# Optimization experiments

Measured on AMD Instinct MI355X. Metric: run time of the kernel, lower is better.

## Reference

```python
import jax, jax.numpy as jnp
import numpy as np
from math import sqrt

MASK_SCALE = 128  # band half-width; entries with |i-j| < MASK_SCALE are masked to -inf

B, L, H, E = 4, 2048, 8, 64
D = 64


def setup_inputs() -> dict:
    key = jax.random.key(0)
    kq, kk, kv = jax.random.split(key, 3)
    queries = jax.random.normal(kq, (B, L, H, E), dtype=jnp.float32)
    keys = jax.random.normal(kk, (B, L, H, E), dtype=jnp.float32)
    values = jax.random.normal(kv, (B, L, H, D), dtype=jnp.float32)
    attn_mask = jnp.zeros((B, 1, L, L), dtype=bool)  # unused (mask_flag=False)
    return {"queries": queries, "keys": keys, "values": values, "attn_mask": attn_mask}


def reference(queries, keys, values, attn_mask):
    b, l, h, e = queries.shape
    scale = 1.0 / sqrt(e)
    # [B,H,L,S] dense scores
    scores = jnp.einsum('blhe,bshe->bhls', queries, keys)
    # create_diag_symmetric_mask(L, MASK_SCALE): 1 iff |i-j| < MASK_SCALE
    idx = jnp.arange(l)
    band = jnp.abs(idx[:, None] - idx[None, :]) < MASK_SCALE  # [L,L]
    # module masks the band to -inf (attends outside the band)
    scores = jnp.where(band[None, None, :, :], -jnp.inf, scores)
    A = jax.nn.softmax(scale * scores, axis=-1)
    V = jnp.einsum('bhls,bshd->blhd', A, values)
    return V
```

## Files before the change

### kernel.cpp

```cpp
#include <hip/hip_runtime.h>
#include <hip/hip_bf16.h>

typedef __bf16 bf16_t;
typedef __bf16 bf16x8 __attribute__((ext_vector_type(8)));
typedef float f32x4 __attribute__((ext_vector_type(4)));
typedef float f32x16 __attribute__((ext_vector_type(16)));
typedef unsigned int u32;

#define MFMA16(A,B,C) __builtin_amdgcn_mfma_f32_16x16x32_bf16(A,B,C,0,0,0)
#define MFMA32(A,B,C) __builtin_amdgcn_mfma_f32_32x32x16_bf16(A,B,C,0,0,0)

constexpr int Bb = 4, Ll = 2048, Hh = 8, Ee = 64, Dd = 64;
constexpr int LDP = 72;
constexpr int MS = 128;

static __device__ __forceinline__ bf16x8 cvt8(float4 a, float4 b) {
    bf16x8 t;
    t[0] = (bf16_t)a.x; t[1] = (bf16_t)a.y; t[2] = (bf16_t)a.z; t[3] = (bf16_t)a.w;
    t[4] = (bf16_t)b.x; t[5] = (bf16_t)b.y; t[6] = (bf16_t)b.z; t[7] = (bf16_t)b.w;
    return t;
}

static __device__ __forceinline__ u32 pkbf(float lo, float hi) {
    u32 d;
    asm("v_cvt_pk_bf16_f32 %0, %1, %2" : "=v"(d) : "v"(lo), "v"(hi));
    return d;
}

static __device__ __forceinline__ float fexp2(float x) {
    float r;
    asm("v_exp_f32 %0, %1" : "=v"(r) : "v"(x));
    return r;
}

static __device__ __forceinline__ f32x16 zero16() {
    f32x16 z;
    #pragma unroll
    for (int r = 0; r < 16; ++r) z[r] = 0.f;
    return z;
}

__global__ __launch_bounds__(256) void cvt_qk(const float* __restrict__ src,
                                              bf16_t* __restrict__ dst,
                                              float scale) {
    const int c = blockIdx.x * 256 + threadIdx.x;
    const int e0 = (c & 7) * 8;
    const int h  = (c >> 3) & (Hh - 1);
    const int l  = (c >> 6) & (Ll - 1);
    const int b  = c >> 17;
    const float* s = src + ((((size_t)b * Ll + l) * Hh + h) * Ee + e0);
    float4 f0 = ((const float4*)s)[0];
    float4 f1 = ((const float4*)s)[1];
    f0.x *= scale; f0.y *= scale; f0.z *= scale; f0.w *= scale;
    f1.x *= scale; f1.y *= scale; f1.z *= scale; f1.w *= scale;
    *(bf16x8*)(dst + ((((size_t)b * Hh + h) * Ll + l) * Ee + e0)) = cvt8(f0, f1);
}

__global__ __launch_bounds__(256) void cvt_v(const float* __restrict__ V,
                                             bf16_t* __restrict__ Vt) {
    __shared__ bf16_t VLp[Dd][LDP];
    const int bh = blockIdx.x >> 5;
    const int t  = blockIdx.x & 31;
    const int b = bh >> 3, h = bh & 7;
    {
        const int j  = threadIdx.x >> 2;
        const int d0 = (threadIdx.x & 3) * 16;
        const float* vp = V + (((size_t)(b * Ll + t * 64 + j)) * Hh + h) * Dd + d0;
        float4 x0 = ((const float4*)vp)[0], x1 = ((const float4*)vp)[1];
        float4 x2 = ((const float4*)vp)[2], x3 = ((const float4*)vp)[3];
        VLp[d0 +  0][j] = (bf16_t)x0.x; VLp[d0 +  1][j] = (bf16_t)x0.y;
        VLp[d0 +  2][j] = (bf16_t)x0.z; VLp[d0 +  3][j] = (bf16_t)x0.w;
        VLp[d0 +  4][j] = (bf16_t)x1.x; VLp[d0 +  5][j] = (bf16_t)x1.y;
        VLp[d0 +  6][j] = (bf16_t)x1.z; VLp[d0 +  7][j] = (bf16_t)x1.w;
        VLp[d0 +  8][j] = (bf16_t)x2.x; VLp[d0 +  9][j] = (bf16_t)x2.y;
        VLp[d0 + 10][j] = (bf16_t)x2.z; VLp[d0 + 11][j] = (bf16_t)x2.w;
        VLp[d0 + 12][j] = (bf16_t)x3.x; VLp[d0 + 13][j] = (bf16_t)x3.y;
        VLp[d0 + 14][j] = (bf16_t)x3.z; VLp[d0 + 15][j] = (bf16_t)x3.w;
    }
    __syncthreads();
    {
        const int d  = threadIdx.x >> 2;
        const int j0 = (threadIdx.x & 3) * 16;
        bf16x8 a0 = *(const bf16x8*)&VLp[d][j0];
        bf16x8 a1 = *(const bf16x8*)&VLp[d][j0 + 8];
        bf16_t* op = Vt + ((((size_t)bh * 32 + t) * 64 + d) * 64 + j0);
        *(bf16x8*)op = a0;
        *(bf16x8*)(op + 8) = a1;
    }
}

__global__ __launch_bounds__(256, 2) void fattn4(const float* __restrict__ Q,
                                                 const bf16_t* __restrict__ Kb,
                                                 const bf16_t* __restrict__ Vt,
                                                 float* __restrict__ O) {
    __shared__ __align__(16) bf16_t KL[2 * 4096];
    __shared__ __align__(16) bf16_t VL[2 * 4096];

    const int tid = threadIdx.x;
    const int wv  = tid >> 6;
    const int ln  = tid & 63;
    const int l31 = ln & 31;
    const int lh  = ln >> 5;

    const int bid = blockIdx.x;
    const int x   = bid & 7;
    const int o   = bid >> 3;
    const int bh  = x * 4 + (o >> 4);
    const int qt  = o & 15;
    const int q0  = qt * 128;
    const int wq0 = q0 + wv * 32;
    const int qq  = wq0 + l31;
    const int b = bh >> 3, h = bh & 7;

    const bf16_t* kbase = Kb + (size_t)bh * (Ll * 64);
    const bf16_t* vbase = Vt + (size_t)bh * (Ll * 64);

    bf16x8 qreg[4];
    {
        const float SCL2 = 0.125f * 1.44269504f;
        const float* qp = Q + (((size_t)(b * Ll + qq)) * Hh + h) * Ee + lh * 8;
        #pragma unroll
        for (int ks = 0; ks < 4; ++ks) {
            float4 f0 = *(const float4*)(qp + ks * 16);
            float4 f1 = *(const float4*)(qp + ks * 16 + 4);
            f0.x *= SCL2; f0.y *= SCL2; f0.z *= SCL2; f0.w *= SCL2;
            f1.x *= SCL2; f1.y *= SCL2; f1.z *= SCL2; f1.w *= SCL2;
            qreg[ks] = cvt8(f0, f1);
        }
    }

    bf16x8 ones;
    #pragma unroll
    for (int e = 0; e < 8; ++e) ones[e] = (bf16_t)1.0f;

    f32x16 acc0 = zero16(), acc1 = zero16(), accP = zero16();

    const int rowoff = (ln >> 3) * 64 + (((ln & 7) ^ (ln >> 3)) * 8);
    const int i0 = (wv & 1) * 4;
    const bf16_t* gsb = (wv < 2) ? kbase : vbase;
    bf16_t* lsb = (wv < 2) ? KL : VL;

    const int s0t = q0 >> 6;
    constexpr int NT = 30;

    #define STAGE(nxt, kt_) do {                                                   \
        const bf16_t* _g = gsb + (kt_) * 4096 + i0 * 512 + rowoff;                 \
        bf16_t* _l = lsb + (nxt) * 4096 + i0 * 512;                                \
        _Pragma("unroll")                                                          \
        for (int _c = 0; _c < 4; ++_c)                                             \
            __builtin_amdgcn_global_load_lds((const void*)(_g + _c * 512),         \
                                             (void*)(_l + _c * 512), 16, 0, 0);    \
    } while (0)

    STAGE(0, (0 >= s0t ? 2 : 0));

    for (int i = 0; i < NT; ++i) {
        const int kt_ = i + (i >= s0t ? 2 : 0);
        const int k0 = kt_ * 64;

        if (i + 1 < NT) {
            STAGE((i + 1) & 1, (i + 1) + ((i + 1) >= s0t ? 2 : 0));
            asm volatile("s_waitcnt vmcnt(4)" ::: "memory");
        } else {
            asm volatile("s_waitcnt vmcnt(0)" ::: "memory");
        }
        __builtin_amdgcn_s_barrier();

        const int bo = (i & 1) * 4096;

        f32x16 s0v = zero16(), s1v = zero16();
        __builtin_amdgcn_s_setprio(1);
        #pragma unroll
        for (int ks = 0; ks < 4; ++ks) {
            const int cc = (((2 * ks + lh) ^ (l31 & 7)) << 3);
            bf16x8 ka0 = *(const bf16x8*)&KL[bo + l31 * 64 + cc];
            bf16x8 ka1 = *(const bf16x8*)&KL[bo + (32 + l31) * 64 + cc];
            s0v = MFMA32(ka0, qreg[ks], s0v);
            s1v = MFMA32(ka1, qreg[ks], s1v);
        }
        __builtin_amdgcn_s_setprio(0);

        {
            const int d0_ = wq0 - k0;
            if (d0_ > -159 && d0_ < 159) {
                #pragma unroll
                for (int r = 0; r < 16; ++r) {
                    const int k = k0 + 4 * lh + ((r & 3) + 8 * (r >> 2));
                    const int dlt = qq - k;
                    if (dlt > -MS && dlt < MS) s0v[r] = -1e30f;
                }
            }
            const int d1_ = wq0 - (k0 + 32);
            if (d1_ > -159 && d1_ < 159) {
                #pragma unroll
                for (int r = 0; r < 16; ++r) {
                    const int k = k0 + 32 + 4 * lh + ((r & 3) + 8 * (r >> 2));
                    const int dlt = qq - k;
                    if (dlt > -MS && dlt < MS) s1v[r] = -1e30f;
                }
            }
        }

        bf16x8 pf[4];
        {
            float p[16];
            #pragma unroll
            for (int r = 0; r < 16; ++r) p[r] = fexp2(s0v[r]);
            u32 x0 = pkbf(p[0], p[1]),   x1 = pkbf(p[2], p[3]);
            u32 x2 = pkbf(p[4], p[5]),   x3 = pkbf(p[6], p[7]);
            u32 x4 = pkbf(p[8], p[9]),   x5 = pkbf(p[10], p[11]);
            u32 x6 = pkbf(p[12], p[13]), x7 = pkbf(p[14], p[15]);
            asm volatile("v_permlane32_swap_b32 %0, %1" : "+v"(x0), "+v"(x2));
            asm volatile("v_permlane32_swap_b32 %0, %1" : "+v"(x1), "+v"(x3));
            asm volatile("v_permlane32_swap_b32 %0, %1" : "+v"(x4), "+v"(x6));
            asm volatile("v_permlane32_swap_b32 %0, %1" : "+v"(x5), "+v"(x7));
            union { u32 w[4]; bf16x8 v; } u0, u1;
            u0.w[0] = x0; u0.w[1] = x1; u0.w[2] = x2; u0.w[3] = x3;
            u1.w[0] = x4; u1.w[1] = x5; u1.w[2] = x6; u1.w[3] = x7;
            pf[0] = u0.v; pf[1] = u1.v;
        }
        {
            float p[16];
            #pragma unroll
            for (int r = 0; r < 16; ++r) p[r] = fexp2(s1v[r]);
            u32 x0 = pkbf(p[0], p[1]),   x1 = pkbf(p[2], p[3]);
            u32 x2 = pkbf(p[4], p[5]),   x3 = pkbf(p[6], p[7]);
            u32 x4 = pkbf(p[8], p[9]),   x5 = pkbf(p[10], p[11]);
            u32 x6 = pkbf(p[12], p[13]), x7 = pkbf(p[14], p[15]);
            asm volatile("v_permlane32_swap_b32 %0, %1" : "+v"(x0), "+v"(x2));
            asm volatile("v_permlane32_swap_b32 %0, %1" : "+v"(x1), "+v"(x3));
            asm volatile("v_permlane32_swap_b32 %0, %1" : "+v"(x4), "+v"(x6));
            asm volatile("v_permlane32_swap_b32 %0, %1" : "+v"(x5), "+v"(x7));
            union { u32 w[4]; bf16x8 v; } u0, u1;
            u0.w[0] = x0; u0.w[1] = x1; u0.w[2] = x2; u0.w[3] = x3;
            u1.w[0] = x4; u1.w[1] = x5; u1.w[2] = x6; u1.w[3] = x7;
            pf[2] = u0.v; pf[3] = u1.v;
        }

        __builtin_amdgcn_s_setprio(1);
        #pragma unroll
        for (int ks = 0; ks < 4; ++ks) {
            const int cc = (((2 * ks + lh) ^ (l31 & 7)) << 3);
            bf16x8 vf0 = *(const bf16x8*)&VL[bo + l31 * 64 + cc];
            bf16x8 vf1 = *(const bf16x8*)&VL[bo + (32 + l31) * 64 + cc];
            acc0 = MFMA32(pf[ks], vf0, acc0);
            acc1 = MFMA32(pf[ks], vf1, acc1);
            accP = MFMA32(pf[ks], ones, accP);
        }
        __builtin_amdgcn_s_setprio(0);

        __builtin_amdgcn_s_barrier();
    }
    #undef STAGE

    #pragma unroll
    for (int r = 0; r < 16; ++r) {
        const int rr = (r & 3) + 8 * (r >> 2) + 4 * lh;
        const float ir = 1.0f / accP[r];
        float* op = O + ((size_t)(b * Ll + wq0 + rr) * Hh + h) * Dd + l31;
        op[0]  = acc0[r] * ir;
        op[32] = acc1[r] * ir;
    }
}

__global__ __launch_bounds__(256, 2) void fattn_f32(const float* __restrict__ Q,
                                                    const float* __restrict__ K,
                                                    const float* __restrict__ V,
                                                    float* __restrict__ O) {
    __shared__ __align__(16) bf16_t Klds[64][LDP];
    __shared__ __align__(16) bf16_t Vtlds[Dd][LDP];
    __shared__ __align__(16) bf16_t Plds[4][16][LDP];

    const int tid = threadIdx.x;
    const int wv  = tid >> 6;
    const int ln  = tid & 63;
    const int l15 = ln & 15;
    const int g   = ln >> 4;

    const int nqt = Ll / 64;
    const int bid = blockIdx.x;
    const int qt  = bid % nqt;
    const int bh  = bid / nqt;
    const int b   = bh >> 3;
    const int h   = bh & 7;
    const int q0  = qt * 64;

    const float SCL2 = 0.125f * 1.44269504f;

    bf16x8 qf[2];
    {
        const float* qp = Q + (((size_t)(b * Ll + q0 + wv * 16 + l15)) * Hh + h) * Ee + g * 8;
        #pragma unroll
        for (int ks = 0; ks < 2; ++ks) {
            float4 f0 = *(const float4*)(qp + 32 * ks);
            float4 f1 = *(const float4*)(qp + 32 * ks + 4);
            qf[ks] = cvt8(f0, f1);
        }
    }

    f32x4 acc[4];
    #pragma unroll
    for (int ct = 0; ct < 4; ++ct) acc[ct] = (f32x4){0.f, 0.f, 0.f, 0.f};
    float m2[4], lsum[4];
    #pragma unroll
    for (int r = 0; r < 4; ++r) { m2[r] = -1e30f; lsum[r] = 0.f; }

    for (int k0 = 0; k0 < Ll; k0 += 64) {
        const int dd = k0 - q0;
        if (dd >= -64 && dd <= 64) continue;
        const bool needmask = (dd == 128) || (dd == -128);

        __syncthreads();
        {
            const int j  = tid >> 2;
            const int c0 = (tid & 3) << 4;
            const float* kp = K + (((size_t)(b * Ll + k0 + j)) * Hh + h) * Ee + c0;
            const float* vp = V + (((size_t)(b * Ll + k0 + j)) * Hh + h) * Dd + c0;
            float4 a0 = ((const float4*)kp)[0], a1 = ((const float4*)kp)[1];
            float4 a2 = ((const float4*)kp)[2], a3 = ((const float4*)kp)[3];
            *(bf16x8*)&Klds[j][c0]     = cvt8(a0, a1);
            *(bf16x8*)&Klds[j][c0 + 8] = cvt8(a2, a3);
            float4 b0 = ((const float4*)vp)[0], b1 = ((const float4*)vp)[1];
            float4 b2 = ((const float4*)vp)[2], b3 = ((const float4*)vp)[3];
            Vtlds[c0 +  0][j] = (bf16_t)b0.x; Vtlds[c0 +  1][j] = (bf16_t)b0.y;
            Vtlds[c0 +  2][j] = (bf16_t)b0.z; Vtlds[c0 +  3][j] = (bf16_t)b0.w;
            Vtlds[c0 +  4][j] = (bf16_t)b1.x; Vtlds[c0 +  5][j] = (bf16_t)b1.y;
            Vtlds[c0 +  6][j] = (bf16_t)b1.z; Vtlds[c0 +  7][j] = (bf16_t)b1.w;
            Vtlds[c0 +  8][j] = (bf16_t)b2.x; Vtlds[c0 +  9][j] = (bf16_t)b2.y;
            Vtlds[c0 + 10][j] = (bf16_t)b2.z; Vtlds[c0 + 11][j] = (bf16_t)b2.w;
            Vtlds[c0 + 12][j] = (bf16_t)b3.x; Vtlds[c0 + 13][j] = (bf16_t)b3.y;
            Vtlds[c0 + 14][j] = (bf16_t)b3.z; Vtlds[c0 + 15][j] = (bf16_t)b3.w;
        }
        __syncthreads();

        f32x4 s[4];
        #pragma unroll
        for (int ct = 0; ct < 4; ++ct) {
            f32x4 z = (f32x4){0.f, 0.f, 0.f, 0.f};
            #pragma unroll
            for (int ks = 0; ks < 2; ++ks) {
                bf16x8 kf = *(const bf16x8*)&Klds[ct * 16 + l15][ks * 32 + g * 8];
                z = MFMA16(qf[ks], kf, z);
            }
            s[ct] = z;
        }

        float lg[4][4];
        #pragma unroll
        for (int ct = 0; ct < 4; ++ct)
            #pragma unroll
            for (int r = 0; r < 4; ++r)
                lg[ct][r] = s[ct][r] * SCL2;

        if (needmask) {
            const int irow = q0 + wv * 16 + g * 4;
            #pragma unroll
            for (int ct = 0; ct < 4; ++ct) {
                const int j = k0 + ct * 16 + l15;
                #pragma unroll
                for (int r = 0; r < 4; ++r) {
                    int diff = irow + r - j;
                    diff = diff < 0 ? -diff : diff;
                    if (diff < MS) lg[ct][r] = -1e30f;
                }
            }
        }

        #pragma unroll
        for (int r = 0; r < 4; ++r) {
            float mx = fmaxf(fmaxf(lg[0][r], lg[1][r]), fmaxf(lg[2][r], lg[3][r]));
            #pragma unroll
            for (int off = 1; off < 16; off <<= 1) mx = fmaxf(mx, __shfl_xor(mx, off));
            const float mnew = fmaxf(m2[r], mx);
            const float c = exp2f(m2[r] - mnew);
            m2[r] = mnew;
            #pragma unroll
            for (int ct = 0; ct < 4; ++ct) acc[ct][r] *= c;
            float ps = 0.f;
            #pragma unroll
            for (int ct = 0; ct < 4; ++ct) {
                float p = exp2f(lg[ct][r] - mnew);
                bf16_t pb = (bf16_t)p;
                Plds[wv][g * 4 + r][ct * 16 + l15] = pb;
                ps += (float)pb;
            }
            #pragma unroll
            for (int off = 1; off < 16; off <<= 1) ps += __shfl_xor(ps, off);
            lsum[r] = lsum[r] * c + ps;
        }

        __syncthreads();

        #pragma unroll
        for (int ks = 0; ks < 2; ++ks) {
            bf16x8 pfr = *(const bf16x8*)&Plds[wv][l15][ks * 32 + g * 8];
            #pragma unroll
            for (int ct = 0; ct < 4; ++ct) {
                bf16x8 vf = *(const bf16x8*)&Vtlds[ct * 16 + l15][ks * 32 + g * 8];
                acc[ct] = MFMA16(pfr, vf, acc[ct]);
            }
        }
    }

    #pragma unroll
    for (int r = 0; r < 4; ++r) {
        const float inv = 1.0f / lsum[r];
        const size_t row = (size_t)(b * Ll + q0 + wv * 16 + g * 4 + r);
        float* op = O + (row * Hh + h) * Dd;
        #pragma unroll
        for (int ct = 0; ct < 4; ++ct)
            op[ct * 16 + l15] = acc[ct][r] * inv;
    }
}

extern "C" void kernel_launch(void* const* d_in, const int* in_sizes, int n_in,
                              void* d_out, int out_size, void* d_ws, size_t ws_size,
                              hipStream_t stream) {
    const float* Q = (const float*)d_in[0];
    const float* K = (const float*)d_in[1];
    const float* V = (const float*)d_in[2];
    float* O = (float*)d_out;

    const size_t nelem = (size_t)Bb * Hh * Ll * Ee;
    const size_t need  = nelem * 2 * 2;

    if (ws_size >= need) {
        bf16_t* Kb = (bf16_t*)d_ws;
        bf16_t* Vt = Kb + nelem;
        cvt_qk<<<dim3(2048), dim3(256), 0, stream>>>(K, Kb, 1.0f);
        cvt_v<<<dim3(Bb * Hh * 32), dim3(256), 0, stream>>>(V, Vt);
        fattn4<<<dim3(512), dim3(256), 0, stream>>>(Q, Kb, Vt, O);
    } else {
        fattn_f32<<<dim3(Bb * Hh * 32), dim3(256), 0, stream>>>(Q, K, V, O);
    }
}
```

Baseline: 62.84 us.

## Share K/V tiles across two query tiles per block and merge prep kernels

```diff
diff --git a/kernel.cpp b/kernel.cpp
--- a/kernel.cpp
+++ b/kernel.cpp
@@ -40,59 +40,58 @@
     return z;
 }
 
-__global__ __launch_bounds__(256) void cvt_qk(const float* __restrict__ src,
-                                              bf16_t* __restrict__ dst,
-                                              float scale) {
-    const int c = blockIdx.x * 256 + threadIdx.x;
-    const int e0 = (c & 7) * 8;
-    const int h  = (c >> 3) & (Hh - 1);
-    const int l  = (c >> 6) & (Ll - 1);
-    const int b  = c >> 17;
-    const float* s = src + ((((size_t)b * Ll + l) * Hh + h) * Ee + e0);
-    float4 f0 = ((const float4*)s)[0];
-    float4 f1 = ((const float4*)s)[1];
-    f0.x *= scale; f0.y *= scale; f0.z *= scale; f0.w *= scale;
-    f1.x *= scale; f1.y *= scale; f1.z *= scale; f1.w *= scale;
-    *(bf16x8*)(dst + ((((size_t)b * Hh + h) * Ll + l) * Ee + e0)) = cvt8(f0, f1);
-}
-
-__global__ __launch_bounds__(256) void cvt_v(const float* __restrict__ V,
-                                             bf16_t* __restrict__ Vt) {
+__global__ __launch_bounds__(256) void prep(const float* __restrict__ K,
+                                            const float* __restrict__ V,
+                                            bf16_t* __restrict__ Kb,
+                                            bf16_t* __restrict__ Vt) {
     __shared__ bf16_t VLp[Dd][LDP];
-    const int bh = blockIdx.x >> 5;
-    const int t  = blockIdx.x & 31;
-    const int b = bh >> 3, h = bh & 7;
-    {
-        const int j  = threadIdx.x >> 2;
-        const int d0 = (threadIdx.x & 3) * 16;
-        const float* vp = V + (((size_t)(b * Ll + t * 64 + j)) * Hh + h) * Dd + d0;
-        float4 x0 = ((const float4*)vp)[0], x1 = ((const float4*)vp)[1];
-        float4 x2 = ((const float4*)vp)[2], x3 = ((const float4*)vp)[3];
-        VLp[d0 +  0][j] = (bf16_t)x0.x; VLp[d0 +  1][j] = (bf16_t)x0.y;
-        VLp[d0 +  2][j] = (bf16_t)x0.z; VLp[d0 +  3][j] = (bf16_t)x0.w;
-        VLp[d0 +  4][j] = (bf16_t)x1.x; VLp[d0 +  5][j] = (bf16_t)x1.y;
-        VLp[d0 +  6][j] = (bf16_t)x1.z; VLp[d0 +  7][j] = (bf16_t)x1.w;
-        VLp[d0 +  8][j] = (bf16_t)x2.x; VLp[d0 +  9][j] = (bf16_t)x2.y;
-        VLp[d0 + 10][j] = (bf16_t)x2.z; VLp[d0 + 11][j] = (bf16_t)x2.w;
-        VLp[d0 + 12][j] = (bf16_t)x3.x; VLp[d0 + 13][j] = (bf16_t)x3.y;
-        VLp[d0 + 14][j] = (bf16_t)x3.z; VLp[d0 + 15][j] = (bf16_t)x3.w;
-    }
-    __syncthreads();
-    {
-        const int d  = threadIdx.x >> 2;
-        const int j0 = (threadIdx.x & 3) * 16;
-        bf16x8 a0 = *(const bf16x8*)&VLp[d][j0];
-        bf16x8 a1 = *(const bf16x8*)&VLp[d][j0 + 8];
-        bf16_t* op = Vt + ((((size_t)bh * 32 + t) * 64 + d) * 64 + j0);
-        *(bf16x8*)op = a0;
-        *(bf16x8*)(op + 8) = a1;
-    }
-}
-
-__global__ __launch_bounds__(256, 2) void fattn4(const float* __restrict__ Q,
-                                                 const bf16_t* __restrict__ Kb,
-                                                 const bf16_t* __restrict__ Vt,
-                                                 float* __restrict__ O) {
+    if (blockIdx.x < 2048) {
+        const int c = blockIdx.x * 256 + threadIdx.x;
+        const int e0 = (c & 7) * 8;
+        const int h  = (c >> 3) & (Hh - 1);
+        const int l  = (c >> 6) & (Ll - 1);
+        const int b  = c >> 17;
+        const float* s = K + ((((size_t)b * Ll + l) * Hh + h) * Ee + e0);
+        float4 f0 = ((const float4*)s)[0];
+        float4 f1 = ((const float4*)s)[1];
+        *(bf16x8*)(Kb + ((((size_t)b * Hh + h) * Ll + l) * Ee + e0)) = cvt8(f0, f1);
+    } else {
+        const int bb = blockIdx.x - 2048;
+        const int bh = bb >> 5;
+        const int t  = bb & 31;
+        const int b = bh >> 3, h = bh & 7;
+        {
+            const int j  = threadIdx.x >> 2;
+            const int d0 = (threadIdx.x & 3) * 16;
+            const float* vp = V + (((size_t)(b * Ll + t * 64 + j)) * Hh + h) * Dd + d0;
+            float4 x0 = ((const float4*)vp)[0], x1 = ((const float4*)vp)[1];
+            float4 x2 = ((const float4*)vp)[2], x3 = ((const float4*)vp)[3];
+            VLp[d0 +  0][j] = (bf16_t)x0.x; VLp[d0 +  1][j] = (bf16_t)x0.y;
+            VLp[d0 +  2][j] = (bf16_t)x0.z; VLp[d0 +  3][j] = (bf16_t)x0.w;
+            VLp[d0 +  4][j] = (bf16_t)x1.x; VLp[d0 +  5][j] = (bf16_t)x1.y;
+            VLp[d0 +  6][j] = (bf16_t)x1.z; VLp[d0 +  7][j] = (bf16_t)x1.w;
+            VLp[d0 +  8][j] = (bf16_t)x2.x; VLp[d0 +  9][j] = (bf16_t)x2.y;
+            VLp[d0 + 10][j] = (bf16_t)x2.z; VLp[d0 + 11][j] = (bf16_t)x2.w;
+            VLp[d0 + 12][j] = (bf16_t)x3.x; VLp[d0 + 13][j] = (bf16_t)x3.y;
+            VLp[d0 + 14][j] = (bf16_t)x3.z; VLp[d0 + 15][j] = (bf16_t)x3.w;
+        }
+        __syncthreads();
+        {
+            const int d  = threadIdx.x >> 2;
+            const int j0 = (threadIdx.x & 3) * 16;
+            bf16x8 a0 = *(const bf16x8*)&VLp[d][j0];
+            bf16x8 a1 = *(const bf16x8*)&VLp[d][j0 + 8];
+            bf16_t* op = Vt + ((((size_t)bh * 32 + t) * 64 + d) * 64 + j0);
+            *(bf16x8*)op = a0;
+            *(bf16x8*)(op + 8) = a1;
+        }
+    }
+}
+
+__global__ __launch_bounds__(512, 1) void fattn10(const float* __restrict__ Q,
+                                                  const bf16_t* __restrict__ Kb,
+                                                  const bf16_t* __restrict__ Vt,
+                                                  float* __restrict__ O) {
     __shared__ __align__(16) bf16_t KL[2 * 4096];
     __shared__ __align__(16) bf16_t VL[2 * 4096];
 
@@ -105,10 +104,10 @@
     const int bid = blockIdx.x;
     const int x   = bid & 7;
     const int o   = bid >> 3;
-    const int bh  = x * 4 + (o >> 4);
-    const int qt  = o & 15;
-    const int q0  = qt * 128;
-    const int wq0 = q0 + wv * 32;
+    const int bh  = x * 4 + (o >> 3);
+    const int p   = o & 7;
+    const int qt  = (wv < 4) ? p : (p + 8);
+    const int wq0 = qt * 128 + (wv & 3) * 32;
     const int qq  = wq0 + l31;
     const int b = bh >> 3, h = bh & 7;
 
@@ -135,32 +134,25 @@
 
     f32x16 acc0 = zero16(), acc1 = zero16(), accP = zero16();
 
-    const int rowoff = (ln >> 3) * 64 + (((ln & 7) ^ (ln >> 3)) * 8);
-    const int i0 = (wv & 1) * 4;
-    const bf16_t* gsb = (wv < 2) ? kbase : vbase;
-    bf16_t* lsb = (wv < 2) ? KL : VL;
-
-    const int s0t = q0 >> 6;
-    constexpr int NT = 30;
+    const int srow = tid >> 3;
+    const int soff = srow * 64 + (((tid & 7) ^ (srow & 7)) << 3);
+    const int ldst = tid * 8;
 
     #define STAGE(nxt, kt_) do {                                                   \
-        const bf16_t* _g = gsb + (kt_) * 4096 + i0 * 512 + rowoff;                 \
-        bf16_t* _l = lsb + (nxt) * 4096 + i0 * 512;                                \
-        _Pragma("unroll")                                                          \
-        for (int _c = 0; _c < 4; ++_c)                                             \
-            __builtin_amdgcn_global_load_lds((const void*)(_g + _c * 512),         \
-                                             (void*)(_l + _c * 512), 16, 0, 0);    \
+        __builtin_amdgcn_global_load_lds((const void*)(kbase + (size_t)(kt_) * 4096\
+                                         + soff), (void*)(KL + (nxt) * 4096 + ldst), 16, 0, 0); \
+        __builtin_amdgcn_global_load_lds((const void*)(vbase + (size_t)(kt_) * 4096\
+                                         + soff), (void*)(VL + (nxt) * 4096 + ldst), 16, 0, 0); \
     } while (0)
 
-    STAGE(0, (0 >= s0t ? 2 : 0));
-
-    for (int i = 0; i < NT; ++i) {
-        const int kt_ = i + (i >= s0t ? 2 : 0);
-        const int k0 = kt_ * 64;
-
-        if (i + 1 < NT) {
-            STAGE((i + 1) & 1, (i + 1) + ((i + 1) >= s0t ? 2 : 0));
-            asm volatile("s_waitcnt vmcnt(4)" ::: "memory");
+    STAGE(0, 0);
+
+    for (int i = 0; i < 32; ++i) {
+        const int k0 = i * 64;
+
+        if (i + 1 < 32) {
+            STAGE((i + 1) & 1, i + 1);
+            asm volatile("s_waitcnt vmcnt(2)" ::: "memory");
         } else {
             asm volatile("s_waitcnt vmcnt(0)" ::: "memory");
         }
@@ -203,13 +195,13 @@
 
         bf16x8 pf[4];
         {
-            float p[16];
-            #pragma unroll
-            for (int r = 0; r < 16; ++r) p[r] = fexp2(s0v[r]);
-            u32 x0 = pkbf(p[0], p[1]),   x1 = pkbf(p[2], p[3]);
-            u32 x2 = pkbf(p[4], p[5]),   x3 = pkbf(p[6], p[7]);
-            u32 x4 = pkbf(p[8], p[9]),   x5 = pkbf(p[10], p[11]);
-            u32 x6 = pkbf(p[12], p[13]), x7 = pkbf(p[14], p[15]);
+            float pp[16];
+            #pragma unroll
+            for (int r = 0; r < 16; ++r) pp[r] = fexp2(s0v[r]);
+            u32 x0 = pkbf(pp[0], pp[1]),   x1 = pkbf(pp[2], pp[3]);
+            u32 x2 = pkbf(pp[4], pp[5]),   x3 = pkbf(pp[6], pp[7]);
+            u32 x4 = pkbf(pp[8], pp[9]),   x5 = pkbf(pp[10], pp[11]);
+            u32 x6 = pkbf(pp[12], pp[13]), x7 = pkbf(pp[14], pp[15]);
             asm volatile("v_permlane32_swap_b32 %0, %1" : "+v"(x0), "+v"(x2));
             asm volatile("v_permlane32_swap_b32 %0, %1" : "+v"(x1), "+v"(x3));
             asm volatile("v_permlane32_swap_b32 %0, %1" : "+v"(x4), "+v"(x6));
@@ -220,13 +212,13 @@
             pf[0] = u0.v; pf[1] = u1.v;
         }
         {
-            float p[16];
-            #pragma unroll
-            for (int r = 0; r < 16; ++r) p[r] = fexp2(s1v[r]);
-            u32 x0 = pkbf(p[0], p[1]),   x1 = pkbf(p[2], p[3]);
-            u32 x2 = pkbf(p[4], p[5]),   x3 = pkbf(p[6], p[7]);
-            u32 x4 = pkbf(p[8], p[9]),   x5 = pkbf(p[10], p[11]);
-            u32 x6 = pkbf(p[12], p[13]), x7 = pkbf(p[14], p[15]);
+            float pp[16];
+            #pragma unroll
+            for (int r = 0; r < 16; ++r) pp[r] = fexp2(s1v[r]);
+            u32 x0 = pkbf(pp[0], pp[1]),   x1 = pkbf(pp[2], pp[3]);
+            u32 x2 = pkbf(pp[4], pp[5]),   x3 = pkbf(pp[6], pp[7]);
+            u32 x4 = pkbf(pp[8], pp[9]),   x5 = pkbf(pp[10], pp[11]);
+            u32 x6 = pkbf(pp[12], pp[13]), x7 = pkbf(pp[14], pp[15]);
             asm volatile("v_permlane32_swap_b32 %0, %1" : "+v"(x0), "+v"(x2));
             asm volatile("v_permlane32_swap_b32 %0, %1" : "+v"(x1), "+v"(x3));
             asm volatile("v_permlane32_swap_b32 %0, %1" : "+v"(x4), "+v"(x6));
@@ -396,8 +388,8 @@
             bf16x8 pfr = *(const bf16x8*)&Plds[wv][l15][ks * 32 + g * 8];
             #pragma unroll
             for (int ct = 0; ct < 4; ++ct) {
-                bf16x8 vf = *(const bf16x8*)&Vtlds[ct * 16 + l15][ks * 32 + g * 8];
-                acc[ct] = MFMA16(pfr, vf, acc[ct]);
+                bf16x8 vfl = *(const bf16x8*)&Vtlds[ct * 16 + l15][ks * 32 + g * 8];
+                acc[ct] = MFMA16(pfr, vfl, acc[ct]);
             }
         }
     }
@@ -427,9 +419,8 @@
     if (ws_size >= need) {
         bf16_t* Kb = (bf16_t*)d_ws;
         bf16_t* Vt = Kb + nelem;
-        cvt_qk<<<dim3(2048), dim3(256), 0, stream>>>(K, Kb, 1.0f);
-        cvt_v<<<dim3(Bb * Hh * 32), dim3(256), 0, stream>>>(V, Vt);
-        fattn4<<<dim3(512), dim3(256), 0, stream>>>(Q, Kb, Vt, O);
+        prep<<<dim3(3072), dim3(256), 0, stream>>>(K, V, Kb, Vt);
+        fattn10<<<dim3(256), dim3(512), 0, stream>>>(Q, Kb, Vt, O);
     } else {
         fattn_f32<<<dim3(Bb * Hh * 32), dim3(256), 0, stream>>>(Q, K, V, O);
     }
```

Measured after the change: 63.34 us. About the same (+0.8%).
